# Kernel tuning notes

Measured on AMD Instinct MI355X. Metric: run time of the kernel, lower is better.

The kernel has to match this reference:

```python
import jax, jax.numpy as jnp
import numpy as np

G = 8           # graphs
NBG = 1024      # blocks per graph
APB = 4         # atoms per block
NC = 1          # coord channels
HID = 512
ES = 64
K = 9
L = 3
NLVL = 50
NB = G * NBG
NU = NB * APB
NUM_BLOCK, NUM_ATOM, NUM_POS = 25, 16, 16
BIG = 1e9


def _cumsum_ids(seg_lengths, n):
    # faithful to torch: zeros, mark segment starts via cumsum(lengths)[:-1], cumsum
    ids = jnp.zeros((n,), jnp.int32).at[jnp.cumsum(seg_lengths)[:-1]].set(1)
    return jnp.cumsum(ids)


def setup_inputs() -> dict:
    key = jax.random.key(0)
    ks = jax.random.split(key, 18)
    s = 0.02
    return {
        'Z': 3.0 * jax.random.normal(ks[0], (NU, NC, 3), jnp.float32),
        'B': jax.random.randint(ks[1], (NB,), 0, NUM_BLOCK),
        'A': jax.random.randint(ks[2], (NU,), 0, NUM_ATOM),
        'atom_positions': jax.random.randint(ks[3], (NU,), 0, NUM_POS),
        'block_lengths': jnp.full((NB,), APB, jnp.int32),
        'lengths': jnp.full((G,), NBG, jnp.int32),
        'segment_ids': jax.random.randint(ks[4], (NB,), 0, 2),
        'noise': jax.random.normal(ks[5], (NU, NC, 3), jnp.float32),
        'noise_level': jax.random.randint(ks[6], (G,), 0, NLVL),
        'sigmas': jnp.asarray(np.exp(np.linspace(np.log(10.0), np.log(0.01), NLVL)), jnp.float32),
        'atom_emb': s * jax.random.normal(ks[7], (NUM_ATOM, HID), jnp.float32),
        'pos_emb': s * jax.random.normal(ks[8], (NUM_POS, HID), jnp.float32),
        'block_emb': s * jax.random.normal(ks[9], (NUM_BLOCK, HID), jnp.float32),
        'edge_emb': s * jax.random.normal(ks[10], (2, ES), jnp.float32),
        'Wm': s * jax.random.normal(ks[11], (L, HID, HID), jnp.float32),
        'We': s * jax.random.normal(ks[12], (L, ES, HID), jnp.float32),
        'Wu': s * jax.random.normal(ks[13], (L, HID, HID), jnp.float32),
        'wz': s * jax.random.normal(ks[14], (L, HID), jnp.float32),
        'W1': s * jax.random.normal(ks[15], (HID, HID), jnp.float32),
        'b1': jnp.zeros((HID,), jnp.float32),
        'W2': s * jax.random.normal(ks[16], (HID, 1), jnp.float32),
    }


def _forward(Z, B, A, atom_positions, block_lengths, lengths, segment_ids,
             noise, noise_level, sigmas, atom_emb, pos_emb, block_emb, edge_emb,
             Wm, We, Wu, wz, W1, b1, W2):
    nb, nu, g = B.shape[0], A.shape[0], lengths.shape[0]
    nbg, apb = nb // g, nu // nb
    batch_id = _cumsum_ids(lengths, nb)        # [Nb]
    block_id = _cumsum_ids(block_lengths, nu)  # [Nu]

    # perturb: Z + noise * sigma[noise_level[graph]]
    used = sigmas[noise_level][batch_id][block_id]          # [Nu]
    Zp = Z + noise * used[:, None, None]                    # [Nu, NC, 3]

    # block embedding: atom + position + block-type
    H0 = atom_emb[A] + pos_emb[atom_positions] + block_emb[B][block_id]  # [Nu, H]

    # edges: fully connect -> split intra/inter by segment -> knn by min atom-pair distance
    xa = Zp.reshape(g, nbg * apb * NC, 3)
    sq = jnp.sum(xa * xa, axis=-1)
    d2 = sq[:, :, None] + sq[:, None, :] - 2.0 * jnp.einsum('gnd,gmd->gnm', xa, xa)
    D = d2.reshape(g, nbg, apb * NC, nbg, apb * NC).min(axis=(2, 4))     # [g, nbg, nbg]
    seg = segment_ids.reshape(g, nbg)
    same = seg[:, :, None] == seg[:, None, :]
    eye = jnp.eye(nbg, dtype=bool)[None]
    _, idx_intra = jax.lax.top_k(-jnp.where(same & ~eye, D, BIG), K)     # [g, nbg, K]
    _, idx_inter = jax.lax.top_k(-jnp.where(~same, D, BIG), K)
    off = (jnp.arange(g, dtype=jnp.int32) * nbg)[:, None, None]
    dst_loc = jnp.broadcast_to(jnp.arange(nbg, dtype=jnp.int32)[None, :, None] + off, (g, nbg, K))
    src = jnp.concatenate([(idx_intra + off).reshape(-1), (idx_inter + off).reshape(-1)])
    dst = jnp.concatenate([dst_loc.reshape(-1), dst_loc.reshape(-1)])
    eattr = edge_emb[jnp.concatenate([jnp.zeros(g * nbg * K, jnp.int32), jnp.ones(g * nbg * K, jnp.int32)])]

    # encoder (GET surrogate): block-level equivariant message passing
    h = jax.ops.segment_sum(H0, block_id, num_segments=nb) / apb                    # [Nb, H]
    Zb0 = jax.ops.segment_sum(Zp.mean(axis=1), block_id, num_segments=nb) / apb    # [Nb, 3]
    Zb = Zb0
    for l in range(Wm.shape[0]):
        m = jax.nn.silu((h[src] + h[dst]) @ Wm[l] + eattr @ We[l])                  # [E, H]
        h = h + jax.nn.silu(jax.ops.segment_sum(m, dst, num_segments=nb) @ Wu[l])
        coef = jnp.tanh(m @ wz[l])                                                  # [E]
        Zb = Zb + jax.ops.segment_sum((Zb[src] - Zb[dst]) * coef[:, None], dst, num_segments=nb) / (2 * K)
    pred_Z = Zp + (Zb - Zb0)[block_id][:, None, :]
    unit_repr = H0 + h[block_id]
    block_repr = h
    graph_repr = jax.ops.segment_sum(h, batch_id, num_segments=g)

    # energy head: SiLU -> Linear -> SiLU -> Linear(no bias), summed per graph
    e = jax.nn.silu(jax.nn.silu(block_repr) @ W1 + b1) @ W2                         # [Nb, 1]
    pred_energy = jax.ops.segment_sum(e[:, 0], batch_id, num_segments=g)            # [g]

    pred_noise = pred_Z - Zp
    per_unit = jnp.sum((pred_noise - noise) ** 2, axis=(-1, -2))                    # [Nu]
    nl = jax.ops.segment_sum(per_unit, batch_id[block_id], num_segments=g)
    loss = 0.5 * nl.mean()
    return pred_energy, pred_noise, unit_repr, block_repr, graph_repr, loss


def reference(Z, B, A, atom_positions, block_lengths, lengths, segment_ids,
              noise, noise_level, sigmas, atom_emb, pos_emb, block_emb, edge_emb,
              Wm, We, Wu, wz, W1, b1, W2):
    return _forward(Z, B, A, atom_positions, block_lengths, lengths, segment_ids,
                    noise, noise_level, sigmas, atom_emb, pos_emb, block_emb, edge_emb,
                    Wm, We, Wu, wz, W1, b1, W2)
```

## Files before the change

### kernel.cpp

```cpp
#include <hip/hip_runtime.h>
#include <hip/hip_bf16.h>

typedef __bf16 bf16;
typedef __bf16 bf16x2 __attribute__((ext_vector_type(2)));
typedef __bf16 bf16x8 __attribute__((ext_vector_type(8)));
typedef float floatx4 __attribute__((ext_vector_type(4)));

#define NB_ 8192
#define NU_ 32768

__device__ __forceinline__ float silu_f(float x) {
    float e = __expf(-x);
    return x * __builtin_amdgcn_rcpf(1.0f + e);
}

__device__ __forceinline__ float2 unpack_bf2(unsigned v) {
    float2 r;
    r.x = __uint_as_float(v << 16);
    r.y = __uint_as_float(v & 0xFFFF0000u);
    return r;
}

__device__ __forceinline__ void gll16(const bf16* g, bf16* l) {
    __builtin_amdgcn_global_load_lds((const __attribute__((address_space(1))) void*)g,
                                     (__attribute__((address_space(3))) void*)l, 16, 0, 0);
}

__device__ __forceinline__ float wave_min_bcast(float v) {
    const int infi = __float_as_int(3.0e38f);
    int vi = __float_as_int(v);
    int t;
    t  = __builtin_amdgcn_update_dpp(infi, vi, 0x111, 0xf, 0xf, false);
    vi = __float_as_int(fminf(__int_as_float(vi), __int_as_float(t)));
    t  = __builtin_amdgcn_update_dpp(infi, vi, 0x112, 0xf, 0xf, false);
    vi = __float_as_int(fminf(__int_as_float(vi), __int_as_float(t)));
    t  = __builtin_amdgcn_update_dpp(infi, vi, 0x114, 0xf, 0xf, false);
    vi = __float_as_int(fminf(__int_as_float(vi), __int_as_float(t)));
    t  = __builtin_amdgcn_update_dpp(infi, vi, 0x118, 0xf, 0xf, false);
    vi = __float_as_int(fminf(__int_as_float(vi), __int_as_float(t)));
    t  = __builtin_amdgcn_update_dpp(infi, vi, 0x142, 0xa, 0xf, false);
    vi = __float_as_int(fminf(__int_as_float(vi), __int_as_float(t)));
    t  = __builtin_amdgcn_update_dpp(infi, vi, 0x143, 0xc, 0xf, false);
    vi = __float_as_int(fminf(__int_as_float(vi), __int_as_float(t)));
    return __int_as_float(__builtin_amdgcn_readlane(vi, 63));
}

__global__ __launch_bounds__(256) void init_kernel(
    const float* __restrict__ Z, const float* __restrict__ noise,
    const int* __restrict__ nl, const float* __restrict__ sig,
    const int* __restrict__ Aarr, const int* __restrict__ posa, const int* __restrict__ Barr,
    const float* __restrict__ atom_emb, const float* __restrict__ pos_emb,
    const float* __restrict__ block_emb,
    const float* __restrict__ edge_emb, const float* __restrict__ We,
    const float* __restrict__ Wm, const float* __restrict__ Wu, const float* __restrict__ W1,
    float* __restrict__ Zp, float* __restrict__ Zb0, float* __restrict__ Zb,
    float* __restrict__ hf, bf16* __restrict__ hb,
    bf16* __restrict__ WmT, bf16* __restrict__ WuT, bf16* __restrict__ W1T,
    float* __restrict__ ebias,
    float* __restrict__ out_gr, float* __restrict__ out_e, float* __restrict__ out_loss)
{
    __shared__ float zsh[12];
    __shared__ float tile[32][33];
    int bid = blockIdx.x, tid = threadIdx.x;
    if (bid < 8192) {
        int b = bid, g = b >> 10;
        if (tid < 12) {
            float sg = sig[nl[g]];
            int idx = b*12 + tid;
            float zp = Z[idx] + noise[idx]*sg;
            Zp[idx] = zp;
            zsh[tid] = zp;
        }
        __syncthreads();
        if (tid < 3) {
            float v = 0.25f*(zsh[tid] + zsh[3+tid] + zsh[6+tid] + zsh[9+tid]);
            Zb0[b*3+tid] = v; Zb[b*3+tid] = v;
        }
        int ai[4], pi[4];
        #pragma unroll
        for (int a = 0; a < 4; a++) { ai[a] = Aarr[b*4+a]*512; pi[a] = posa[b*4+a]*512; }
        int bb = Barr[b]*512;
        #pragma unroll
        for (int cc = 0; cc < 2; cc++) {
            int c = tid + cc*256;
            float s = 0.0f;
            #pragma unroll
            for (int a = 0; a < 4; a++) s += atom_emb[ai[a]+c] + pos_emb[pi[a]+c];
            s = 0.25f*s + block_emb[bb+c];
            hf[(size_t)b*512+c] = s;
            hb[(size_t)b*512+c] = (bf16)s;
        }
        return;
    }
    bid -= 8192;
    if (bid < 1792) {
        int z = bid >> 8, rem = bid & 255;
        int bx = rem & 15, by = rem >> 4;
        int tx = tid & 31, ty = tid >> 5;
        const float* src; bf16* dst;
        if (z < 3)      { src = Wm + (size_t)z*262144;     dst = WmT + (size_t)z*262144; }
        else if (z < 6) { src = Wu + (size_t)(z-3)*262144; dst = WuT + (size_t)(z-3)*262144; }
        else            { src = W1;                        dst = W1T; }
        #pragma unroll
        for (int i = 0; i < 32; i += 8)
            tile[ty+i][tx] = src[(size_t)(by*32+ty+i)*512 + bx*32+tx];
        __syncthreads();
        #pragma unroll
        for (int i = 0; i < 32; i += 8)
            dst[(size_t)(bx*32+ty+i)*512 + by*32+tx] = (bf16)tile[tx][ty+i];
        return;
    }
    bid -= 1792;
    if (bid < 12) {
        int gid = bid*256 + tid;
        int l = gid >> 10, t = (gid >> 9) & 1, c = gid & 511;
        float s = 0.0f;
        #pragma unroll 8
        for (int e = 0; e < 64; e++)
            s += edge_emb[t*64 + e] * We[(size_t)(l*64 + e)*512 + c];
        ebias[gid] = s;
        return;
    }
    bid -= 12;
    int k = bid*256 + tid;
    if (k < 4096) out_gr[k] = 0.0f;
    else if (k < 4104) out_e[k-4096] = 0.0f;
    else if (k == 4104) out_loss[0] = 0.0f;
}

__device__ void knn_body(int kb, const float* __restrict__ Zp, const int* __restrict__ seg,
                         int* __restrict__ nbr) {
    int wid = threadIdx.x >> 6;
    int lane = threadIdx.x & 63;
    int r = ((kb & 7) << 10) + ((kb >> 3) << 2) + wid;
    int g = r >> 10;
    int il = r & 1023;
    int base = g << 10;
    int segr = seg[r];
    float za[4][3];
    #pragma unroll
    for (int a = 0; a < 4; a++)
        #pragma unroll
        for (int d = 0; d < 3; d++)
            za[a][d] = Zp[r*12 + a*3 + d];
    float dist[16];
    unsigned smask = 0;
    #pragma unroll
    for (int t = 0; t < 16; t++) {
        int jb = base + t*64 + lane;
        const float4* p = (const float4*)(Zp + (size_t)jb*12);
        float4 v0 = p[0], v1 = p[1], v2 = p[2];
        float bx[4] = {v0.x, v0.w, v1.z, v2.y};
        float by[4] = {v0.y, v1.x, v1.w, v2.z};
        float bz[4] = {v0.z, v1.y, v2.x, v2.w};
        float dm = 3.0e38f;
        #pragma unroll
        for (int a = 0; a < 4; a++) {
            #pragma unroll
            for (int bq = 0; bq < 4; bq++) {
                float dx = za[a][0]-bx[bq], dy = za[a][1]-by[bq], dz = za[a][2]-bz[bq];
                dm = fminf(dm, dx*dx + dy*dy + dz*dz);
            }
        }
        dist[t] = dm;
        if (seg[jb] == segr) smask |= (1u << t);
    }
    const float INF = 3.0e38f;
    for (int phase = 0; phase < 2; phase++) {
        float wd[16];
        #pragma unroll
        for (int t = 0; t < 16; t++) {
            bool ok = (phase == 0) ? (((smask >> t) & 1u) && (t*64 + lane != il))
                                   : (!((smask >> t) & 1u));
            wd[t] = ok ? dist[t] : INF;
        }
        for (int it = 0; it < 9; it++) {
            float a0 = fminf(fminf(wd[0],  wd[1]),  wd[2]);
            float a1 = fminf(fminf(wd[3],  wd[4]),  wd[5]);
            float a2 = fminf(fminf(wd[6],  wd[7]),  wd[8]);
            float a3 = fminf(fminf(wd[9],  wd[10]), wd[11]);
            float a4 = fminf(fminf(wd[12], wd[13]), wd[14]);
            float b0 = fminf(fminf(a0, a1), a2);
            float b1v = fminf(fminf(a3, a4), wd[15]);
            float mv = wave_min_bcast(fminf(b0, b1v));
            int wt = -1; unsigned long long wm = 0ull;
            #pragma unroll
            for (int t = 0; t < 16; t++) {
                unsigned long long bm = __ballot(wd[t] == mv);
                bool take = (wt < 0) && (bm != 0ull);
                wt = take ? t : wt;
                wm = take ? bm : wm;
            }
            int wl = __ffsll(wm) - 1;
            if (lane == 0) nbr[r*18 + phase*9 + it] = base + wt*64 + wl;
            bool mine = (lane == wl);
            #pragma unroll
            for (int t = 0; t < 16; t++)
                if (t == wt && mine) wd[t] = INF;
        }
    }
}

__device__ void gemm_body(const bf16* __restrict__ A, const bf16* __restrict__ BT,
                          bf16* __restrict__ Pb, float* __restrict__ hf,
                          bf16* __restrict__ hb, bf16* __restrict__ shp,
                          const float* __restrict__ b1, const float* __restrict__ W2,
                          float* __restrict__ out_e,
                          float* __restrict__ Zb, const float* __restrict__ zacc,
                          int mode, int bid)
{
    __shared__ alignas(16) bf16 sA[128*32];
    __shared__ alignas(16) bf16 sB[64*32];
    int mt = bid & 63, nt = bid >> 6;
    int m0 = mt*128, n0 = nt*64;
    int tid = threadIdx.x, lane = tid & 63, w = tid >> 6;
    int wm = w & 1, wn = w >> 1;
    int lm = lane & 15, q = lane >> 4;

    int pA0 = w*128 + lane, pA1 = pA0 + 64, pB = w*64 + lane;
    int rA0 = pA0 >> 2, qA0 = (pA0 & 3) ^ ((rA0 >> 1) & 3);
    int rA1 = pA1 >> 2, qA1 = (pA1 & 3) ^ ((rA1 >> 1) & 3);
    int rB  = pB  >> 2, qB  = (pB  & 3) ^ ((rB  >> 1) & 3);
    const bf16* gA0 = A  + (size_t)(m0 + rA0)*512 + qA0*8;
    const bf16* gA1 = A  + (size_t)(m0 + rA1)*512 + qA1*8;
    const bf16* gB  = BT + (size_t)(n0 + rB )*512 + qB*8;
    bf16* lA0 = sA + (w*128)*8;
    bf16* lA1 = sA + (w*128 + 64)*8;
    bf16* lB  = sB + (w*64)*8;

    int swq = (q ^ ((lm >> 1) & 3)) * 8;
    const bf16* pa[4]; const bf16* pb2[2];
    #pragma unroll
    for (int tm = 0; tm < 4; tm++) pa[tm] = sA + (wm*64 + tm*16 + lm)*32 + swq;
    #pragma unroll
    for (int tn = 0; tn < 2; tn++) pb2[tn] = sB + (wn*32 + tn*16 + lm)*32 + swq;

    floatx4 zv = {0.0f, 0.0f, 0.0f, 0.0f};
    floatx4 acc[4][2];
    #pragma unroll
    for (int i = 0; i < 4; i++)
        #pragma unroll
        for (int j = 0; j < 2; j++) acc[i][j] = zv;

    for (int k0 = 0; k0 < 512; k0 += 32) {
        gll16(gA0 + k0, lA0);
        gll16(gA1 + k0, lA1);
        gll16(gB  + k0, lB);
        __syncthreads();
        bf16x8 af[4], bfr[2];
        #pragma unroll
        for (int tm = 0; tm < 4; tm++) af[tm] = *(const bf16x8*)pa[tm];
        #pragma unroll
        for (int tn = 0; tn < 2; tn++) bfr[tn] = *(const bf16x8*)pb2[tn];
        #pragma unroll
        for (int tm = 0; tm < 4; tm++)
            #pragma unroll
            for (int tn = 0; tn < 2; tn++)
                acc[tm][tn] = __builtin_amdgcn_mfma_f32_16x16x32_bf16(af[tm], bfr[tn], acc[tm][tn], 0, 0, 0);
        __syncthreads();
    }

    if (mode == 1 && nt == 0) {
        int o = m0*3 + tid;
        Zb[o] += zacc[o] * (1.0f/18.0f);
        if (tid < 128) {
            int o2 = m0*3 + 256 + tid;
            Zb[o2] += zacc[o2] * (1.0f/18.0f);
        }
    }

    if (mode == 2) {
        float esum = 0.0f;
        #pragma unroll
        for (int tn = 0; tn < 2; tn++) {
            int col = n0 + wn*32 + tn*16 + lm;
            float bb = b1[col];
            float w2 = W2[col];
            #pragma unroll
            for (int tm = 0; tm < 4; tm++)
                #pragma unroll
                for (int rr = 0; rr < 4; rr++)
                    esum += silu_f(acc[tm][tn][rr] + bb) * w2;
        }
        #pragma unroll
        for (int off = 32; off >= 1; off >>= 1) esum += __shfl_xor(esum, off, 64);
        __shared__ float ered[4];
        if (lane == 0) ered[w] = esum;
        __syncthreads();
        if (tid == 0) {
            float tot = ered[0] + ered[1] + ered[2] + ered[3];
            atomicAdd(&out_e[m0 >> 10], tot);
        }
        return;
    }
    #pragma unroll
    for (int tm = 0; tm < 4; tm++) {
        #pragma unroll
        for (int tn = 0; tn < 2; tn++) {
            #pragma unroll
            for (int rr = 0; rr < 4; rr++) {
                int row = m0 + wm*64 + tm*16 + q*4 + rr;
                int col = n0 + wn*32 + tn*16 + lm;
                size_t o = (size_t)row*512 + col;
                float v = acc[tm][tn][rr];
                if (mode == 0) {
                    Pb[o] = (bf16)v;
                } else {
                    float nh = hf[o] + silu_f(v);
                    hf[o] = nh;
                    hb[o] = (bf16)nh;
                    if (shp) shp[o] = (bf16)silu_f(nh);
                }
            }
        }
    }
}

__global__ __launch_bounds__(256) void gemm_kernel(const bf16* __restrict__ A, const bf16* __restrict__ BT,
                                                   bf16* __restrict__ Pb, float* __restrict__ hf,
                                                   bf16* __restrict__ hb, bf16* __restrict__ shp,
                                                   const float* __restrict__ b1, const float* __restrict__ W2,
                                                   float* __restrict__ out_e,
                                                   float* __restrict__ Zb, const float* __restrict__ zacc,
                                                   int mode) {
    gemm_body(A, BT, Pb, hf, hb, shp, b1, W2, out_e, Zb, zacc, mode, blockIdx.x);
}

__global__ __launch_bounds__(256) void knn_pgemm0_kernel(const bf16* __restrict__ hb,
                                                         const bf16* __restrict__ WmT0,
                                                         bf16* __restrict__ Pb,
                                                         const float* __restrict__ Zp,
                                                         const int* __restrict__ seg,
                                                         int* __restrict__ nbr) {
    if (blockIdx.x < 512)
        gemm_body(hb, WmT0, Pb, nullptr, nullptr, nullptr, nullptr, nullptr, nullptr,
                  nullptr, nullptr, 0, blockIdx.x);
    else
        knn_body(blockIdx.x - 512, Zp, seg, nbr);
}

__global__ __launch_bounds__(256) void edge_kernel(const bf16* __restrict__ Pb, const float* __restrict__ ebias,
                                                   const float* __restrict__ wz, const float* __restrict__ Zb,
                                                   const int* __restrict__ nbr, bf16* __restrict__ msum,
                                                   float* __restrict__ zacc) {
    int bid = blockIdx.x, tid = threadIdx.x;
    int b = ((bid & 7) << 10) | (bid >> 3);
    int c0 = 2*tid;
    int lane = tid & 63, wid = tid >> 6;
    __shared__ int srcs[18];
    __shared__ float red[18][4];
    __shared__ float term[18][3];
    if (tid < 18) srcs[tid] = nbr[b*18 + tid];
    __syncthreads();
    float2 pd  = unpack_bf2(*(const unsigned*)(Pb + (size_t)b*512 + c0));
    float2 eb0 = *(const float2*)(ebias + c0);
    float2 eb1 = *(const float2*)(ebias + 512 + c0);
    float2 w   = *(const float2*)(wz + c0);
    float ms0 = 0.0f, ms1 = 0.0f;
    float pdot[18];
    #pragma unroll
    for (int e = 0; e < 18; e++) {
        int s = srcs[e];
        float2 pv = unpack_bf2(*(const unsigned*)(Pb + (size_t)s*512 + c0));
        float ba = (e < 9) ? eb0.x : eb1.x;
        float bb = (e < 9) ? eb0.y : eb1.y;
        float m0 = silu_f(pv.x + pd.x + ba);
        float m1 = silu_f(pv.y + pd.y + bb);
        ms0 += m0; ms1 += m1;
        pdot[e] = m0*w.x + m1*w.y;
    }
    bf16x2 mp = { (bf16)ms0, (bf16)ms1 };
    *(bf16x2*)(msum + (size_t)b*512 + c0) = mp;
    #pragma unroll
    for (int e = 0; e < 18; e++) {
        float v = pdot[e];
        #pragma unroll
        for (int off = 32; off >= 1; off >>= 1) v += __shfl_xor(v, off, 64);
        if (lane == 0) red[e][wid] = v;
    }
    __syncthreads();
    if (tid < 18) {
        float dot = red[tid][0] + red[tid][1] + red[tid][2] + red[tid][3];
        float coef = tanhf(dot);
        int s = srcs[tid];
        #pragma unroll
        for (int d = 0; d < 3; d++)
            term[tid][d] = (Zb[s*3 + d] - Zb[b*3 + d]) * coef;
    }
    __syncthreads();
    if (tid < 3) {
        float s = 0.0f;
        #pragma unroll
        for (int e = 0; e < 18; e++) s += term[e][tid];
        zacc[b*3 + tid] = s;
    }
}

__global__ __launch_bounds__(256) void finalize_kernel(const float* __restrict__ hf, float* __restrict__ out_gr,
                                                       const float* __restrict__ Zb, const float* __restrict__ Zb0,
                                                       const float* __restrict__ noise,
                                                       float* __restrict__ out_pn, float* __restrict__ out_loss) {
    __shared__ float red[256];
    int bid = blockIdx.x, tid = threadIdx.x;
    if (bid < 128) {
        int u = bid*256 + tid;
        int b = u >> 2;
        float per = 0.0f;
        #pragma unroll
        for (int d = 0; d < 3; d++) {
            float dv = Zb[b*3+d] - Zb0[b*3+d];
            out_pn[u*3+d] = dv;
            float e = dv - noise[u*3+d];
            per += e*e;
        }
        red[tid] = per; __syncthreads();
        for (int st = 128; st > 0; st >>= 1) {
            if (tid < st) red[tid] += red[tid+st];
            __syncthreads();
        }
        if (tid == 0) atomicAdd(out_loss, red[0] * (1.0f/16.0f));
        return;
    }
    int pid = bid - 128;
    int g = pid >> 5;
    int rc = (pid >> 1) & 15;
    int ch = pid & 1;
    int c = ch*256 + tid;
    int b0 = (g << 10) + rc*64;
    float s = 0.0f;
    for (int i = 0; i < 64; i++) s += hf[(size_t)(b0+i)*512 + c];
    atomicAdd(&out_gr[g*512 + c], s);
}

__global__ __launch_bounds__(256) void unitrepr_kernel(const int* __restrict__ Aarr, const int* __restrict__ posa,
                                                       const int* __restrict__ Barr,
                                                       const float* __restrict__ atom_emb, const float* __restrict__ pos_emb,
                                                       const float* __restrict__ block_emb,
                                                       const float* __restrict__ hf, float* __restrict__ out_ur) {
    int gid = blockIdx.x*256 + threadIdx.x;
    int u = gid >> 7, c = (gid & 127) << 2, b = u >> 2;
    float4 va = *(const float4*)(atom_emb + (size_t)Aarr[u]*512 + c);
    float4 vp = *(const float4*)(pos_emb + (size_t)posa[u]*512 + c);
    float4 vb = *(const float4*)(block_emb + (size_t)Barr[b]*512 + c);
    float4 vh = *(const float4*)(hf + (size_t)b*512 + c);
    float4 o;
    o.x = va.x + vp.x + vb.x + vh.x;
    o.y = va.y + vp.y + vb.y + vh.y;
    o.z = va.z + vp.z + vb.z + vh.z;
    o.w = va.w + vp.w + vb.w + vh.w;
    *(float4*)(out_ur + (size_t)u*512 + c) = o;
}

extern "C" void kernel_launch(void* const* d_in, const int* in_sizes, int n_in,
                              void* d_out, int out_size, void* d_ws, size_t ws_size,
                              hipStream_t stream) {
    const float* Z         = (const float*)d_in[0];
    const int*   B         = (const int*)d_in[1];
    const int*   A         = (const int*)d_in[2];
    const int*   ap        = (const int*)d_in[3];
    const int*   seg       = (const int*)d_in[6];
    const float* noise     = (const float*)d_in[7];
    const int*   nl        = (const int*)d_in[8];
    const float* sig       = (const float*)d_in[9];
    const float* atom_emb  = (const float*)d_in[10];
    const float* pos_emb   = (const float*)d_in[11];
    const float* block_emb = (const float*)d_in[12];
    const float* edge_emb  = (const float*)d_in[13];
    const float* Wm        = (const float*)d_in[14];
    const float* We        = (const float*)d_in[15];
    const float* Wu        = (const float*)d_in[16];
    const float* wz        = (const float*)d_in[17];
    const float* W1        = (const float*)d_in[18];
    const float* b1        = (const float*)d_in[19];
    const float* W2        = (const float*)d_in[20];
    (void)in_sizes; (void)n_in; (void)d_ws; (void)ws_size; (void)out_size;

    float* out = (float*)d_out;
    const size_t o1 = 8, o2 = 98312, o3 = 16875528, o4 = 21069832, o5 = 21073928;
    float* out_e    = out;
    float* out_pn   = out + o1;
    float* out_ur   = out + o2;
    float* hf       = out + o3;
    float* out_gr   = out + o4;
    float* out_loss = out + o5;

    char* arena = (char*)(out + o2);
    bf16*  Pb   = (bf16*)(arena);
    bf16*  msum = (bf16*)(arena + 16777216);
    bf16*  sh   = (bf16*)(arena + 25165824);
    bf16*  hb   = (bf16*)(arena + 33554432);
    float* Zp   = (float*)(arena + 41943040);
    float* Zb0  = (float*)(arena + 42336256);
    float* Zb   = (float*)(arena + 42434560);
    float* zacc = (float*)(arena + 42532864);
    int*   nbr  = (int*)  (arena + 42631168);
    bf16*  WmT  = (bf16*) (arena + 43220992);
    bf16*  WuT  = (bf16*) (arena + 44793856);
    bf16*  W1T  = (bf16*) (arena + 46366720);
    float* ebias= (float*)(arena + 46891008);

    init_kernel<<<8192 + 1792 + 12 + 17, 256, 0, stream>>>(
        Z, noise, nl, sig, A, ap, B, atom_emb, pos_emb, block_emb,
        edge_emb, We, Wm, Wu, W1,
        Zp, Zb0, Zb, hf, hb, WmT, WuT, W1T, ebias, out_gr, out_e, out_loss);

    knn_pgemm0_kernel<<<512 + 2048, 256, 0, stream>>>(hb, WmT, Pb, Zp, seg, nbr);

    for (int l = 0; l < 3; l++) {
        if (l > 0)
            gemm_kernel<<<512, 256, 0, stream>>>(hb, WmT + (size_t)l*262144, Pb,
                                                 nullptr, nullptr, nullptr, nullptr, nullptr, nullptr,
                                                 nullptr, nullptr, 0);
        edge_kernel<<<8192, 256, 0, stream>>>(Pb, ebias + l*1024, wz + l*512, Zb, nbr, msum, zacc);
        gemm_kernel<<<512, 256, 0, stream>>>(msum, WuT + (size_t)l*262144, nullptr,
                                             hf, hb, (l == 2) ? sh : nullptr, nullptr, nullptr, nullptr,
                                             Zb, zacc, 1);
    }
    gemm_kernel<<<512, 256, 0, stream>>>(sh, W1T, nullptr, nullptr, nullptr, nullptr,
                                         b1, W2, out_e, nullptr, nullptr, 2);
    finalize_kernel<<<384, 256, 0, stream>>>(hf, out_gr, Zb, Zb0, noise, out_pn, out_loss);
    unitrepr_kernel<<<16384, 256, 0, stream>>>(A, ap, B, atom_emb, pos_emb, block_emb, hf, out_ur);
}
```

Before: 505.8 us.

## Double-buffer LDS in standalone GEMM and simplify kNN argmin selection

The standalone GEMM kernel now double-buffers its LDS tiles, issuing the next K-slice's global-to-LDS loads before the MFMAs on the current slice. This halves the barriers per iteration and is meant to hide load latency. The fused kNN+GEMM kernel keeps the single-buffer path. Separately, the kNN selection loop now finds each lane's local argmin over 16 slots, then does a shuffle-xor min, one ballot and a lane shuffle, replacing 16 ballots per iteration. Risks: double buffering doubles shared memory, which may lower occupancy, and tie-breaking order in the kNN selection may differ.

After: 491.5 us. -2.8%, faster.

```diff
diff --git a/kernel.cpp b/kernel.cpp
--- a/kernel.cpp
+++ b/kernel.cpp
@@ -24,25 +24,6 @@
 __device__ __forceinline__ void gll16(const bf16* g, bf16* l) {
     __builtin_amdgcn_global_load_lds((const __attribute__((address_space(1))) void*)g,
                                      (__attribute__((address_space(3))) void*)l, 16, 0, 0);
-}
-
-__device__ __forceinline__ float wave_min_bcast(float v) {
-    const int infi = __float_as_int(3.0e38f);
-    int vi = __float_as_int(v);
-    int t;
-    t  = __builtin_amdgcn_update_dpp(infi, vi, 0x111, 0xf, 0xf, false);
-    vi = __float_as_int(fminf(__int_as_float(vi), __int_as_float(t)));
-    t  = __builtin_amdgcn_update_dpp(infi, vi, 0x112, 0xf, 0xf, false);
-    vi = __float_as_int(fminf(__int_as_float(vi), __int_as_float(t)));
-    t  = __builtin_amdgcn_update_dpp(infi, vi, 0x114, 0xf, 0xf, false);
-    vi = __float_as_int(fminf(__int_as_float(vi), __int_as_float(t)));
-    t  = __builtin_amdgcn_update_dpp(infi, vi, 0x118, 0xf, 0xf, false);
-    vi = __float_as_int(fminf(__int_as_float(vi), __int_as_float(t)));
-    t  = __builtin_amdgcn_update_dpp(infi, vi, 0x142, 0xa, 0xf, false);
-    vi = __float_as_int(fminf(__int_as_float(vi), __int_as_float(t)));
-    t  = __builtin_amdgcn_update_dpp(infi, vi, 0x143, 0xc, 0xf, false);
-    vi = __float_as_int(fminf(__int_as_float(vi), __int_as_float(t)));
-    return __int_as_float(__builtin_amdgcn_readlane(vi, 63));
 }
 
 __global__ __launch_bounds__(256) void init_kernel(
@@ -175,32 +156,24 @@
             wd[t] = ok ? dist[t] : INF;
         }
         for (int it = 0; it < 9; it++) {
-            float a0 = fminf(fminf(wd[0],  wd[1]),  wd[2]);
-            float a1 = fminf(fminf(wd[3],  wd[4]),  wd[5]);
-            float a2 = fminf(fminf(wd[6],  wd[7]),  wd[8]);
-            float a3 = fminf(fminf(wd[9],  wd[10]), wd[11]);
-            float a4 = fminf(fminf(wd[12], wd[13]), wd[14]);
-            float b0 = fminf(fminf(a0, a1), a2);
-            float b1v = fminf(fminf(a3, a4), wd[15]);
-            float mv = wave_min_bcast(fminf(b0, b1v));
-            int wt = -1; unsigned long long wm = 0ull;
-            #pragma unroll
-            for (int t = 0; t < 16; t++) {
-                unsigned long long bm = __ballot(wd[t] == mv);
-                bool take = (wt < 0) && (bm != 0ull);
-                wt = take ? t : wt;
-                wm = take ? bm : wm;
-            }
-            int wl = __ffsll(wm) - 1;
+            float bd = wd[0]; int bt = 0;
+            #pragma unroll
+            for (int t = 1; t < 16; t++) { if (wd[t] < bd) { bd = wd[t]; bt = t; } }
+            float mv = bd;
+            #pragma unroll
+            for (int off = 32; off >= 1; off >>= 1) mv = fminf(mv, __shfl_xor(mv, off, 64));
+            unsigned long long msk = __ballot(bd == mv);
+            int wl = __ffsll(msk) - 1;
+            int wt = __shfl(bt, wl, 64);
             if (lane == 0) nbr[r*18 + phase*9 + it] = base + wt*64 + wl;
-            bool mine = (lane == wl);
-            #pragma unroll
-            for (int t = 0; t < 16; t++)
-                if (t == wt && mine) wd[t] = INF;
-        }
-    }
-}
-
+            bool amwin = (lane == wl);
+            #pragma unroll
+            for (int t = 0; t < 16; t++) if (amwin && t == wt) wd[t] = INF;
+        }
+    }
+}
+
+template<int DB>
 __device__ void gemm_body(const bf16* __restrict__ A, const bf16* __restrict__ BT,
                           bf16* __restrict__ Pb, float* __restrict__ hf,
                           bf16* __restrict__ hb, bf16* __restrict__ shp,
@@ -209,8 +182,8 @@
                           float* __restrict__ Zb, const float* __restrict__ zacc,
                           int mode, int bid)
 {
-    __shared__ alignas(16) bf16 sA[128*32];
-    __shared__ alignas(16) bf16 sB[64*32];
+    __shared__ alignas(16) bf16 sA[(DB+1)*128*32];
+    __shared__ alignas(16) bf16 sB[(DB+1)*64*32];
     int mt = bid & 63, nt = bid >> 6;
     int m0 = mt*128, n0 = nt*64;
     int tid = threadIdx.x, lane = tid & 63, w = tid >> 6;
@@ -224,16 +197,14 @@
     const bf16* gA0 = A  + (size_t)(m0 + rA0)*512 + qA0*8;
     const bf16* gA1 = A  + (size_t)(m0 + rA1)*512 + qA1*8;
     const bf16* gB  = BT + (size_t)(n0 + rB )*512 + qB*8;
-    bf16* lA0 = sA + (w*128)*8;
-    bf16* lA1 = sA + (w*128 + 64)*8;
-    bf16* lB  = sB + (w*64)*8;
+    int dA0 = (w*128)*8, dA1 = (w*128 + 64)*8, dB = (w*64)*8;
 
     int swq = (q ^ ((lm >> 1) & 3)) * 8;
-    const bf16* pa[4]; const bf16* pb2[2];
-    #pragma unroll
-    for (int tm = 0; tm < 4; tm++) pa[tm] = sA + (wm*64 + tm*16 + lm)*32 + swq;
-    #pragma unroll
-    for (int tn = 0; tn < 2; tn++) pb2[tn] = sB + (wn*32 + tn*16 + lm)*32 + swq;
+    int offA[4], offB[2];
+    #pragma unroll
+    for (int tm = 0; tm < 4; tm++) offA[tm] = (wm*64 + tm*16 + lm)*32 + swq;
+    #pragma unroll
+    for (int tn = 0; tn < 2; tn++) offB[tn] = (wn*32 + tn*16 + lm)*32 + swq;
 
     floatx4 zv = {0.0f, 0.0f, 0.0f, 0.0f};
     floatx4 acc[4][2];
@@ -242,22 +213,52 @@
         #pragma unroll
         for (int j = 0; j < 2; j++) acc[i][j] = zv;
 
-    for (int k0 = 0; k0 < 512; k0 += 32) {
-        gll16(gA0 + k0, lA0);
-        gll16(gA1 + k0, lA1);
-        gll16(gB  + k0, lB);
+    if constexpr (DB == 0) {
+        for (int k0 = 0; k0 < 512; k0 += 32) {
+            gll16(gA0 + k0, sA + dA0);
+            gll16(gA1 + k0, sA + dA1);
+            gll16(gB  + k0, sB + dB);
+            __syncthreads();
+            bf16x8 af[4], bfr[2];
+            #pragma unroll
+            for (int tm = 0; tm < 4; tm++) af[tm] = *(const bf16x8*)(sA + offA[tm]);
+            #pragma unroll
+            for (int tn = 0; tn < 2; tn++) bfr[tn] = *(const bf16x8*)(sB + offB[tn]);
+            #pragma unroll
+            for (int tm = 0; tm < 4; tm++)
+                #pragma unroll
+                for (int tn = 0; tn < 2; tn++)
+                    acc[tm][tn] = __builtin_amdgcn_mfma_f32_16x16x32_bf16(af[tm], bfr[tn], acc[tm][tn], 0, 0, 0);
+            __syncthreads();
+        }
+    } else {
+        gll16(gA0, sA + dA0);
+        gll16(gA1, sA + dA1);
+        gll16(gB,  sB + dB);
         __syncthreads();
-        bf16x8 af[4], bfr[2];
-        #pragma unroll
-        for (int tm = 0; tm < 4; tm++) af[tm] = *(const bf16x8*)pa[tm];
-        #pragma unroll
-        for (int tn = 0; tn < 2; tn++) bfr[tn] = *(const bf16x8*)pb2[tn];
-        #pragma unroll
-        for (int tm = 0; tm < 4; tm++)
-            #pragma unroll
-            for (int tn = 0; tn < 2; tn++)
-                acc[tm][tn] = __builtin_amdgcn_mfma_f32_16x16x32_bf16(af[tm], bfr[tn], acc[tm][tn], 0, 0, 0);
-        __syncthreads();
+        for (int t = 0; t < 16; t++) {
+            int cur = t & 1;
+            if (t < 15) {
+                int k0 = (t + 1) * 32;
+                int nb = cur ^ 1;
+                gll16(gA0 + k0, sA + nb*4096 + dA0);
+                gll16(gA1 + k0, sA + nb*4096 + dA1);
+                gll16(gB  + k0, sB + nb*2048 + dB);
+            }
+            const bf16* a_ = sA + cur*4096;
+            const bf16* b_ = sB + cur*2048;
+            bf16x8 af[4], bfr[2];
+            #pragma unroll
+            for (int tm = 0; tm < 4; tm++) af[tm] = *(const bf16x8*)(a_ + offA[tm]);
+            #pragma unroll
+            for (int tn = 0; tn < 2; tn++) bfr[tn] = *(const bf16x8*)(b_ + offB[tn]);
+            #pragma unroll
+            for (int tm = 0; tm < 4; tm++)
+                #pragma unroll
+                for (int tn = 0; tn < 2; tn++)
+                    acc[tm][tn] = __builtin_amdgcn_mfma_f32_16x16x32_bf16(af[tm], bfr[tn], acc[tm][tn], 0, 0, 0);
+            __syncthreads();
+        }
     }
 
     if (mode == 1 && nt == 0) {
@@ -323,7 +324,7 @@
                                                    float* __restrict__ out_e,
                                                    float* __restrict__ Zb, const float* __restrict__ zacc,
                                                    int mode) {
-    gemm_body(A, BT, Pb, hf, hb, shp, b1, W2, out_e, Zb, zacc, mode, blockIdx.x);
+    gemm_body<1>(A, BT, Pb, hf, hb, shp, b1, W2, out_e, Zb, zacc, mode, blockIdx.x);
 }
 
 __global__ __launch_bounds__(256) void knn_pgemm0_kernel(const bf16* __restrict__ hb,
@@ -333,8 +334,8 @@
                                                          const int* __restrict__ seg,
                                                          int* __restrict__ nbr) {
     if (blockIdx.x < 512)
-        gemm_body(hb, WmT0, Pb, nullptr, nullptr, nullptr, nullptr, nullptr, nullptr,
-                  nullptr, nullptr, 0, blockIdx.x);
+        gemm_body<0>(hb, WmT0, Pb, nullptr, nullptr, nullptr, nullptr, nullptr, nullptr,
+                     nullptr, nullptr, 0, blockIdx.x);
     else
         knn_body(blockIdx.x - 512, Zp, seg, nbr);
 }
```
